# Kernel optimization log

Hardware: AMD Instinct MI355X
Metric: run time of the kernel (lower is better)

The kernel has to match this reference:

```python
import jax, jax.numpy as jnp
import numpy as np

TEMPERATURE = 0.07
EPS = 1e-12  # matches F.normalize eps

def _l2norm(x, axis):
    n = jnp.sqrt(jnp.sum(x * x, axis=axis, keepdims=True))
    return x / jnp.maximum(n, EPS)

def setup_inputs() -> dict:
    key = jax.random.key(0)
    features = jax.random.normal(key, (512, 256), dtype=jnp.float32)
    return {"features": features}

def reference(features) -> jnp.ndarray:
    B = features.shape[0]
    f = _l2norm(features, axis=1)                      # [B, D]
    fi = f[:, None, :]                                 # broadcast over j
    fj = f[None, :, :]                                 # broadcast over i
    mutual = fi * fj                                   # [B, B, D]
    gate_i = fi * mutual
    gate_j = fj * mutual
    # torch broadcasting: + features adds f[j, k] along trailing dims
    feats_self_i = _l2norm(fi * gate_i + f, axis=2)
    feats_other_i = _l2norm(fi * gate_j + f, axis=2)
    feats_other_j = _l2norm(fj * gate_i + f, axis=2)
    # note: features_self_j is computed in the original but never used in any dot product

    raw_self_i = jnp.einsum('ik,ijk->ij', f, feats_self_i) / TEMPERATURE
    raw_self_j = jnp.einsum('ik,ijk->ij', f, feats_other_j) / TEMPERATURE  # (original uses other_j here)
    raw_other_i = jnp.einsum('ik,ijk->ij', f, feats_other_i) / TEMPERATURE
    raw_other_j = jnp.einsum('ik,ijk->ij', f, feats_other_j) / TEMPERATURE

    logits_mask = 1.0 - jnp.eye(B, dtype=f.dtype)      # zero out diagonal
    exp_sum = (jnp.exp(raw_self_i) + jnp.exp(raw_self_j)
               + jnp.exp(raw_other_i) + jnp.exp(raw_other_j)) * logits_mask
    vs_all = jnp.sum(exp_sum, axis=1, keepdims=True)   # [B, 1]

    log_prob = raw_self_i - jnp.log(vs_all)            # [B, B]
    mean_log_prob_pos = jnp.sum(log_prob, axis=1) / B
    loss = -jnp.mean(mean_log_prob_pos)
    return loss
```

## Files before the change

kernel.cpp:

```cpp
#include <hip/hip_runtime.h>
#include <math.h>

#define Bq 512
#define Dq 256

__device__ __forceinline__ float waveReduceSum(float v) {
    #pragma unroll
    for (int off = 32; off > 0; off >>= 1)
        v += __shfl_xor(v, off, 64);
    return v;
}

__global__ __launch_bounds__(256) void prep_kernel(
        const float* __restrict__ feat,
        float* __restrict__ fT, float* __restrict__ C1, float* __restrict__ C2,
        float* __restrict__ A1, float* __restrict__ A2) {
    int i = blockIdx.x;
    int k = threadIdx.x;
    float x = feat[i * Dq + k];
    float ss = waveReduceSum(x * x);
    __shared__ float wsum[4];
    int wid = threadIdx.x >> 6, lane = threadIdx.x & 63;
    if (lane == 0) wsum[wid] = ss;
    __syncthreads();
    float tot = wsum[0] + wsum[1] + wsum[2] + wsum[3];
    float n = fmaxf(sqrtf(tot), 1e-12f);
    float a = x / n;
    float a2 = a * a;
    float a3 = a2 * a;
    float c0 = 1.0f + a3;
    fT[k * Bq + i] = a;
    A1[i * Dq + k] = a;
    A2[i * Dq + k] = a2;
    C1[i * Dq + k] = a * c0;
    C2[i * Dq + k] = c0 * c0;
}

__global__ __launch_bounds__(512) void pair_kernel(
        const float* __restrict__ fT,
        const float* __restrict__ C1, const float* __restrict__ C2,
        const float* __restrict__ A1, const float* __restrict__ A2,
        float* __restrict__ Sv, float* __restrict__ Vv) {
    int i = blockIdx.x;
    int j = threadIdx.x;
    const float* __restrict__ c1 = C1 + i * Dq;
    const float* __restrict__ c2 = C2 + i * Dq;
    const float* __restrict__ a1 = A1 + i * Dq;
    const float* __restrict__ a2p = A2 + i * Dq;

    float du = 0.f, nu = 0.f, dv = 0.f, nv = 0.f;
    #pragma unroll 8
    for (int k = 0; k < Dq; ++k) {
        float b  = fT[k * Bq + j];
        float b2 = b * b;
        float w  = fmaf(a2p[k], b, 1.0f);
        float wb = w * b;
        du = fmaf(c1[k], b,  du);
        nu = fmaf(c2[k], b2, nu);
        dv = fmaf(a1[k], wb, dv);
        nv = fmaf(wb,    wb, nv);
    }
    const float Tinv = 1.0f / 0.07f;
    float raw_s = du / fmaxf(sqrtf(nu), 1e-12f) * Tinv;
    float raw_o = dv / fmaxf(sqrtf(nv), 1e-12f) * Tinv;

    float sS = raw_s;
    float sV = (j == i) ? 0.0f : (expf(raw_s) + 3.0f * expf(raw_o));

    sS = waveReduceSum(sS);
    sV = waveReduceSum(sV);
    __shared__ float redS[8], redV[8];
    int wid = threadIdx.x >> 6, lane = threadIdx.x & 63;
    if (lane == 0) { redS[wid] = sS; redV[wid] = sV; }
    __syncthreads();
    if (threadIdx.x == 0) {
        float S = 0.f, V = 0.f;
        #pragma unroll
        for (int w2 = 0; w2 < 8; ++w2) { S += redS[w2]; V += redV[w2]; }
        Sv[i] = S;
        Vv[i] = V;
    }
}

__global__ __launch_bounds__(512) void final_kernel(
        const float* __restrict__ Sv, const float* __restrict__ Vv,
        float* __restrict__ out) {
    int i = threadIdx.x;
    float t = Sv[i] * (1.0f / Bq) - logf(Vv[i]);
    t = waveReduceSum(t);
    __shared__ float red[8];
    int wid = i >> 6, lane = i & 63;
    if (lane == 0) red[wid] = t;
    __syncthreads();
    if (i == 0) {
        float s = 0.f;
        #pragma unroll
        for (int w = 0; w < 8; ++w) s += red[w];
        out[0] = -s / (float)Bq;
    }
}

extern "C" void kernel_launch(void* const* d_in, const int* in_sizes, int n_in,
                              void* d_out, int out_size, void* d_ws, size_t ws_size,
                              hipStream_t stream) {
    const float* feat = (const float*)d_in[0];
    float* ws = (float*)d_ws;
    float* fT = ws;
    float* C1 = fT + Bq * Dq;
    float* C2 = C1 + Bq * Dq;
    float* A1 = C2 + Bq * Dq;
    float* A2 = A1 + Bq * Dq;
    float* Sv = A2 + Bq * Dq;
    float* Vv = Sv + Bq;

    prep_kernel<<<Bq, Dq, 0, stream>>>(feat, fT, C1, C2, A1, A2);
    pair_kernel<<<Bq, Bq, 0, stream>>>(fT, C1, C2, A1, A2, Sv, Vv);
    final_kernel<<<1, Bq, 0, stream>>>(Sv, Vv, (float*)d_out);
}
```

Before: 82.23 us.

## Stage row coefficients in LDS and compute two columns per thread

The pair kernel now copies the four per-row coefficient vectors into shared memory and reads them as float4. Each thread handles two adjacent j columns through a float2 load of fT, and the block size drops from 512 to 256 threads. This is meant to cut redundant global and scalar coefficient loads and to reuse each coefficient across two columns. The cost is more registers per thread and fewer waves per block.

Result: faster. 77.35 us (-5.9%).

```diff
diff --git a/kernel.cpp b/kernel.cpp
--- a/kernel.cpp
+++ b/kernel.cpp
@@ -36,47 +36,91 @@
     C2[i * Dq + k] = c0 * c0;
 }
 
-__global__ __launch_bounds__(512) void pair_kernel(
+__global__ __launch_bounds__(256) void pair_kernel(
         const float* __restrict__ fT,
         const float* __restrict__ C1, const float* __restrict__ C2,
         const float* __restrict__ A1, const float* __restrict__ A2,
         float* __restrict__ Sv, float* __restrict__ Vv) {
-    int i = blockIdx.x;
-    int j = threadIdx.x;
-    const float* __restrict__ c1 = C1 + i * Dq;
-    const float* __restrict__ c2 = C2 + i * Dq;
-    const float* __restrict__ a1 = A1 + i * Dq;
-    const float* __restrict__ a2p = A2 + i * Dq;
+    const int i = blockIdx.x;
+    const int t = threadIdx.x;
+    const int j0 = 2 * t;
 
-    float du = 0.f, nu = 0.f, dv = 0.f, nv = 0.f;
-    #pragma unroll 8
-    for (int k = 0; k < Dq; ++k) {
-        float b  = fT[k * Bq + j];
-        float b2 = b * b;
-        float w  = fmaf(a2p[k], b, 1.0f);
-        float wb = w * b;
-        du = fmaf(c1[k], b,  du);
-        nu = fmaf(c2[k], b2, nu);
-        dv = fmaf(a1[k], wb, dv);
-        nv = fmaf(wb,    wb, nv);
+    __shared__ __align__(16) float s_c1[Dq];
+    __shared__ __align__(16) float s_c2[Dq];
+    __shared__ __align__(16) float s_a1[Dq];
+    __shared__ __align__(16) float s_a2[Dq];
+    s_c1[t] = C1[i * Dq + t];
+    s_c2[t] = C2[i * Dq + t];
+    s_a1[t] = A1[i * Dq + t];
+    s_a2[t] = A2[i * Dq + t];
+    __syncthreads();
+
+    const float4* __restrict__ vc1 = (const float4*)s_c1;
+    const float4* __restrict__ vc2 = (const float4*)s_c2;
+    const float4* __restrict__ va1 = (const float4*)s_a1;
+    const float4* __restrict__ va2 = (const float4*)s_a2;
+
+    float du0 = 0.f, nu0 = 0.f, dv0 = 0.f, nv0 = 0.f;
+    float du1 = 0.f, nu1 = 0.f, dv1 = 0.f, nv1 = 0.f;
+
+    #pragma unroll 4
+    for (int k4 = 0; k4 < Dq / 4; ++k4) {
+        float4 c1 = vc1[k4];
+        float4 c2 = vc2[k4];
+        float4 a1 = va1[k4];
+        float4 a2 = va2[k4];
+        const float c1a[4] = {c1.x, c1.y, c1.z, c1.w};
+        const float c2a[4] = {c2.x, c2.y, c2.z, c2.w};
+        const float a1a[4] = {a1.x, a1.y, a1.z, a1.w};
+        const float a2a[4] = {a2.x, a2.y, a2.z, a2.w};
+        #pragma unroll
+        for (int kk = 0; kk < 4; ++kk) {
+            int k = k4 * 4 + kk;
+            float2 b2v = *(const float2*)(fT + k * Bq + j0);
+            {
+                float b = b2v.x;
+                float bb = b * b;
+                float w  = fmaf(a2a[kk], b, 1.0f);
+                float wb = w * b;
+                du0 = fmaf(c1a[kk], b,  du0);
+                nu0 = fmaf(c2a[kk], bb, nu0);
+                dv0 = fmaf(a1a[kk], wb, dv0);
+                nv0 = fmaf(wb,      wb, nv0);
+            }
+            {
+                float b = b2v.y;
+                float bb = b * b;
+                float w  = fmaf(a2a[kk], b, 1.0f);
+                float wb = w * b;
+                du1 = fmaf(c1a[kk], b,  du1);
+                nu1 = fmaf(c2a[kk], bb, nu1);
+                dv1 = fmaf(a1a[kk], wb, dv1);
+                nv1 = fmaf(wb,      wb, nv1);
+            }
+        }
     }
+
     const float Tinv = 1.0f / 0.07f;
-    float raw_s = du / fmaxf(sqrtf(nu), 1e-12f) * Tinv;
-    float raw_o = dv / fmaxf(sqrtf(nv), 1e-12f) * Tinv;
+    float raw_s0 = du0 / fmaxf(sqrtf(nu0), 1e-12f) * Tinv;
+    float raw_o0 = dv0 / fmaxf(sqrtf(nv0), 1e-12f) * Tinv;
+    float raw_s1 = du1 / fmaxf(sqrtf(nu1), 1e-12f) * Tinv;
+    float raw_o1 = dv1 / fmaxf(sqrtf(nv1), 1e-12f) * Tinv;
 
-    float sS = raw_s;
-    float sV = (j == i) ? 0.0f : (expf(raw_s) + 3.0f * expf(raw_o));
+    float sS = raw_s0 + raw_s1;
+    float sV = 0.f;
+    if (j0 != i)     sV += expf(raw_s0) + 3.0f * expf(raw_o0);
+    if (j0 + 1 != i) sV += expf(raw_s1) + 3.0f * expf(raw_o1);
 
     sS = waveReduceSum(sS);
     sV = waveReduceSum(sV);
-    __shared__ float redS[8], redV[8];
-    int wid = threadIdx.x >> 6, lane = threadIdx.x & 63;
+    __shared__ float redS[4], redV[4];
+    int wid = t >> 6, lane = t & 63;
     if (lane == 0) { redS[wid] = sS; redV[wid] = sV; }
     __syncthreads();
-    if (threadIdx.x == 0) {
+    if (t == 0) {
         float S = 0.f, V = 0.f;
         #pragma unroll
-        for (int w2 = 0; w2 < 8; ++w2) { S += redS[w2]; V += redV[w2]; }
+        for (int w2 = 0; w2 < 4; ++w2) { S += redS[w2]; V += redV[w2]; }
         Sv[i] = S;
         Vv[i] = V;
     }
@@ -114,6 +158,6 @@
     float* Vv = Sv + Bq;
 
     prep_kernel<<<Bq, Dq, 0, stream>>>(feat, fT, C1, C2, A1, A2);
-    pair_kernel<<<Bq, Bq, 0, stream>>>(fT, C1, C2, A1, A2, Sv, Vv);
+    pair_kernel<<<Bq, 256, 0, stream>>>(fT, C1, C2, A1, A2, Sv, Vv);
     final_kernel<<<1, Bq, 0, stream>>>(Sv, Vv, (float*)d_out);
 }
```

## Register-block pair kernel 2x2 with shared-memory row operands and float2 loads

Applied to the files above, without the earlier changes.

Each block of the pair kernel now handles two rows i and 256 threads, with each thread computing a 2x2 tile of (i,j) pairs. Row operands are staged in shared memory and read as float4, and column values are loaded as float2, so every loaded element feeds more FMAs. The prep kernel stores one c0 array instead of the precomputed C1 and C2; the pair kernel recomputes those terms per pair, which adds some arithmetic. The per-row log term is moved into the pair kernel, leaving the final kernel as a plain sum. The grid is halved to 256 blocks, which may leave part of the GPU idle.

After: 79.18 us. 3.7% less time.

```diff
diff --git a/kernel.cpp b/kernel.cpp
--- a/kernel.cpp
+++ b/kernel.cpp
@@ -13,8 +13,8 @@
 
 __global__ __launch_bounds__(256) void prep_kernel(
         const float* __restrict__ feat,
-        float* __restrict__ fT, float* __restrict__ C1, float* __restrict__ C2,
-        float* __restrict__ A1, float* __restrict__ A2) {
+        float* __restrict__ fT, float* __restrict__ A1,
+        float* __restrict__ A2, float* __restrict__ C0) {
     int i = blockIdx.x;
     int k = threadIdx.x;
     float x = feat[i * Dq + k];
@@ -27,67 +27,106 @@
     float n = fmaxf(sqrtf(tot), 1e-12f);
     float a = x / n;
     float a2 = a * a;
-    float a3 = a2 * a;
-    float c0 = 1.0f + a3;
+    float c0 = 1.0f + a2 * a;
     fT[k * Bq + i] = a;
     A1[i * Dq + k] = a;
     A2[i * Dq + k] = a2;
-    C1[i * Dq + k] = a * c0;
-    C2[i * Dq + k] = c0 * c0;
+    C0[i * Dq + k] = c0;
 }
 
-__global__ __launch_bounds__(512) void pair_kernel(
+__global__ __launch_bounds__(256) void pair_kernel(
         const float* __restrict__ fT,
-        const float* __restrict__ C1, const float* __restrict__ C2,
         const float* __restrict__ A1, const float* __restrict__ A2,
-        float* __restrict__ Sv, float* __restrict__ Vv) {
-    int i = blockIdx.x;
-    int j = threadIdx.x;
-    const float* __restrict__ c1 = C1 + i * Dq;
-    const float* __restrict__ c2 = C2 + i * Dq;
-    const float* __restrict__ a1 = A1 + i * Dq;
-    const float* __restrict__ a2p = A2 + i * Dq;
+        const float* __restrict__ C0,
+        float* __restrict__ Tv) {
+    const int i0 = blockIdx.x * 2;
+    const int t = threadIdx.x;
+    const int j0 = 2 * t;
 
-    float du = 0.f, nu = 0.f, dv = 0.f, nv = 0.f;
-    #pragma unroll 8
-    for (int k = 0; k < Dq; ++k) {
-        float b  = fT[k * Bq + j];
-        float b2 = b * b;
-        float w  = fmaf(a2p[k], b, 1.0f);
-        float wb = w * b;
-        du = fmaf(c1[k], b,  du);
-        nu = fmaf(c2[k], b2, nu);
-        dv = fmaf(a1[k], wb, dv);
-        nv = fmaf(wb,    wb, nv);
+    __shared__ __align__(16) float s_a[2][Dq];
+    __shared__ __align__(16) float s_q[2][Dq];
+    __shared__ __align__(16) float s_c[2][Dq];
+    #pragma unroll
+    for (int r = 0; r < 2; ++r) {
+        s_a[r][t] = A1[(i0 + r) * Dq + t];
+        s_q[r][t] = A2[(i0 + r) * Dq + t];
+        s_c[r][t] = C0[(i0 + r) * Dq + t];
     }
+    __syncthreads();
+
+    float du[2][2] = {{0.f,0.f},{0.f,0.f}};
+    float nu[2][2] = {{0.f,0.f},{0.f,0.f}};
+    float dv[2][2] = {{0.f,0.f},{0.f,0.f}};
+    float nv[2][2] = {{0.f,0.f},{0.f,0.f}};
+
+    const float* __restrict__ pb = fT + j0;
+
+    #pragma unroll 2
+    for (int k4 = 0; k4 < Dq / 4; ++k4) {
+        float4 a4[2], q4[2], c4[2];
+        #pragma unroll
+        for (int r = 0; r < 2; ++r) {
+            a4[r] = ((const float4*)s_a[r])[k4];
+            q4[r] = ((const float4*)s_q[r])[k4];
+            c4[r] = ((const float4*)s_c[r])[k4];
+        }
+        #pragma unroll
+        for (int kk = 0; kk < 4; ++kk) {
+            const int k = k4 * 4 + kk;
+            float2 bv = *(const float2*)(pb + k * Bq);
+            const float aa[2] = { ((const float*)&a4[0])[kk], ((const float*)&a4[1])[kk] };
+            const float qq[2] = { ((const float*)&q4[0])[kk], ((const float*)&q4[1])[kk] };
+            const float cc[2] = { ((const float*)&c4[0])[kk], ((const float*)&c4[1])[kk] };
+            const float bs[2] = { bv.x, bv.y };
+            #pragma unroll
+            for (int jj = 0; jj < 2; ++jj) {
+                float b  = bs[jj];
+                float bb = b * b;
+                #pragma unroll
+                for (int ii = 0; ii < 2; ++ii) {
+                    float g  = cc[ii] * b;
+                    float wb = fmaf(qq[ii], bb, b);
+                    du[ii][jj] = fmaf(aa[ii], g,  du[ii][jj]);
+                    nu[ii][jj] = fmaf(g,      g,  nu[ii][jj]);
+                    dv[ii][jj] = fmaf(aa[ii], wb, dv[ii][jj]);
+                    nv[ii][jj] = fmaf(wb,     wb, nv[ii][jj]);
+                }
+            }
+        }
+    }
+
     const float Tinv = 1.0f / 0.07f;
-    float raw_s = du / fmaxf(sqrtf(nu), 1e-12f) * Tinv;
-    float raw_o = dv / fmaxf(sqrtf(nv), 1e-12f) * Tinv;
+    __shared__ float redS[2][4], redV[2][4];
+    const int wid = t >> 6, lane = t & 63;
 
-    float sS = raw_s;
-    float sV = (j == i) ? 0.0f : (expf(raw_s) + 3.0f * expf(raw_o));
-
-    sS = waveReduceSum(sS);
-    sV = waveReduceSum(sV);
-    __shared__ float redS[8], redV[8];
-    int wid = threadIdx.x >> 6, lane = threadIdx.x & 63;
-    if (lane == 0) { redS[wid] = sS; redV[wid] = sV; }
+    #pragma unroll
+    for (int ii = 0; ii < 2; ++ii) {
+        const int i = i0 + ii;
+        float sS = 0.f, sV = 0.f;
+        #pragma unroll
+        for (int jj = 0; jj < 2; ++jj) {
+            const int j = j0 + jj;
+            float raw_s = du[ii][jj] / fmaxf(sqrtf(nu[ii][jj]), 1e-12f) * Tinv;
+            float raw_o = dv[ii][jj] / fmaxf(sqrtf(nv[ii][jj]), 1e-12f) * Tinv;
+            sS += raw_s;
+            if (j != i) sV += expf(raw_s) + 3.0f * expf(raw_o);
+        }
+        sS = waveReduceSum(sS);
+        sV = waveReduceSum(sV);
+        if (lane == 0) { redS[ii][wid] = sS; redV[ii][wid] = sV; }
+    }
     __syncthreads();
-    if (threadIdx.x == 0) {
-        float S = 0.f, V = 0.f;
-        #pragma unroll
-        for (int w2 = 0; w2 < 8; ++w2) { S += redS[w2]; V += redV[w2]; }
-        Sv[i] = S;
-        Vv[i] = V;
+    if (t < 2) {
+        float S = redS[t][0] + redS[t][1] + redS[t][2] + redS[t][3];
+        float V = redV[t][0] + redV[t][1] + redV[t][2] + redV[t][3];
+        Tv[i0 + t] = S * (1.0f / Bq) - logf(V);
     }
 }
 
 __global__ __launch_bounds__(512) void final_kernel(
-        const float* __restrict__ Sv, const float* __restrict__ Vv,
-        float* __restrict__ out) {
+        const float* __restrict__ Tv, float* __restrict__ out) {
     int i = threadIdx.x;
-    float t = Sv[i] * (1.0f / Bq) - logf(Vv[i]);
-    t = waveReduceSum(t);
+    float t = waveReduceSum(Tv[i]);
     __shared__ float red[8];
     int wid = i >> 6, lane = i & 63;
     if (lane == 0) red[wid] = t;
@@ -106,14 +145,12 @@
     const float* feat = (const float*)d_in[0];
     float* ws = (float*)d_ws;
     float* fT = ws;
-    float* C1 = fT + Bq * Dq;
-    float* C2 = C1 + Bq * Dq;
-    float* A1 = C2 + Bq * Dq;
-    float* A2 = A1 + Bq * Dq;
-    float* Sv = A2 + Bq * Dq;
-    float* Vv = Sv + Bq;
+    float* A1 = fT + (size_t)Bq * Dq;
+    float* A2 = A1 + (size_t)Bq * Dq;
+    float* C0 = A2 + (size_t)Bq * Dq;
+    float* Tv = C0 + (size_t)Bq * Dq;
 
-    prep_kernel<<<Bq, Dq, 0, stream>>>(feat, fT, C1, C2, A1, A2);
-    pair_kernel<<<Bq, Bq, 0, stream>>>(fT, C1, C2, A1, A2, Sv, Vv);
-    final_kernel<<<1, Bq, 0, stream>>>(Sv, Vv, (float*)d_out);
+    prep_kernel<<<Bq, Dq, 0, stream>>>(feat, fT, A1, A2, C0);
+    pair_kernel<<<Bq / 2, 256, 0, stream>>>(fT, A1, A2, C0, Tv);
+    final_kernel<<<1, Bq, 0, stream>>>(Tv, (float*)d_out);
 }
```
